# Performance work log

Measured on AMD Instinct MI355X. Metric: run time of the kernel, lower is better.

The kernel has to match this reference:

```python
import jax, jax.numpy as jnp
import numpy as np
import math

IMAGE_SIZE = 256
N_ANGLES = 180


def setup_inputs() -> dict:
    key = jax.random.key(0)
    x = jax.random.normal(key, (4, 1, IMAGE_SIZE, IMAGE_SIZE), dtype=jnp.float32)
    return {"x": x}


def reference(x) -> jnp.ndarray:
    # Radon transform, circle=True: mask to inscribed circle, then for each
    # angle bilinearly sample the image along rotated coordinates
    # (torch.grid_sample, align_corners=True, zeros padding) and sum along rays.
    B = x.shape[0]
    S = IMAGE_SIZE
    A = N_ANGLES
    img = x.reshape(B, S, S)

    # circular mask (matches torch: sqrt(dist2) <= center with center = S//2)
    center = S // 2
    yy, xx = jnp.meshgrid(jnp.arange(S), jnp.arange(S), indexing='ij')
    dist = jnp.sqrt(((xx - center) ** 2 + (yy - center) ** 2).astype(jnp.float32))
    img = img * (dist <= center).astype(img.dtype)
    img_flat = img.reshape(B, S * S)

    # projection coordinates: meshgrid('ij') of linspace(-S/2, S/2, S)
    lin = jnp.linspace(-S / 2.0, S / 2.0, S, dtype=jnp.float32)
    X, Y = jnp.meshgrid(lin, lin, indexing='ij')  # [S,S]; X varies along i
    Xf, Yf = X.ravel(), Y.ravel()                 # [S*S]

    # all rotation angles at once: torch.linspace(0, 180, A) degrees
    ang = jnp.linspace(0.0, 180.0, A, dtype=jnp.float32) * (math.pi / 180.0)
    c = jnp.cos(ang)[:, None]  # [A,1]
    s = jnp.sin(ang)[:, None]
    half = S / 2.0
    gx = (c * Xf - s * Yf) / half  # [A, S*S], normalized grid x (width)
    gy = (s * Xf + c * Yf) / half  # [A, S*S], normalized grid y (height)

    # align_corners=True: pixel = (g + 1)/2 * (S - 1)
    px = (gx + 1.0) * 0.5 * (S - 1)
    py = (gy + 1.0) * 0.5 * (S - 1)

    x0 = jnp.floor(px)
    y0 = jnp.floor(py)
    wx = px - x0
    wy = py - y0
    x0i = x0.astype(jnp.int32)
    y0i = y0.astype(jnp.int32)
    x1i = x0i + 1
    y1i = y0i + 1

    def corner(xi, yi, w):
        # zeros padding: out-of-bounds corners contribute 0
        valid = (xi >= 0) & (xi < S) & (yi >= 0) & (yi < S)
        idx = jnp.clip(yi, 0, S - 1) * S + jnp.clip(xi, 0, S - 1)  # [A, S*S]
        vals = jnp.take(img_flat, idx, axis=1)                      # [B, A, S*S]
        return vals * (w * valid.astype(img.dtype))

    acc = (corner(x0i, y0i, (1.0 - wx) * (1.0 - wy))
           + corner(x1i, y0i, wx * (1.0 - wy))
           + corner(x0i, y1i, (1.0 - wx) * wy)
           + corner(x1i, y1i, wx * wy))  # [B, A, S*S]

    # flat order is (i, j) from meshgrid('ij'); torch sums over output H == i
    sinogram = acc.reshape(B, A, S, S).sum(axis=2)  # [B, A, S]
    return sinogram
```

## Files before the change

### kernel.cpp

```cpp
#include <hip/hip_runtime.h>
#include <hip/hip_fp16.h>
#include <math.h>

#define S 256
#define A 180
#define B 4
#define NSLOT 18285

__global__ void radon_mask_pack(const float* __restrict__ in, uint* __restrict__ ws,
                                float* __restrict__ osino) {
    int idx = blockIdx.x * 256 + threadIdx.x;
    if (idx < 2 * S * S) {
        int c = idx >> 16;
        int p = idx & 65535;
        int y = p >> 8;
        int x = p & 255;
        int dx = x - 128, dy = y - 128;
        bool inside = (dx * dx + dy * dy <= 16384);
        float v0 = in[(2 * c) * (S * S) + p];
        float v1 = in[(2 * c + 1) * (S * S) + p];
        v0 = inside ? v0 : 0.0f;
        v1 = inside ? v1 : 0.0f;
        uint lo = (uint)__half_as_ushort(__float2half(v0));
        uint hi = (uint)__half_as_ushort(__float2half(v1));
        ws[c * (S * S) + p] = lo | (hi << 16);
    }
    if (idx < A * B * S) osino[idx] = 0.0f;
}

__global__ __launch_bounds__(1024, 8) void radon_lds_kernel(const uint* __restrict__ ws,
                                                            float* __restrict__ out) {
    __shared__ uint lds[NSLOT];

    const int a = blockIdx.x;
    const int c = blockIdx.y;
    const int g = blockIdx.z;
    const int tid = threadIdx.x;

    float ang = (float)a * (float)(M_PI / 179.0);
    float sn, cs;
    sincosf(ang, &sn, &cs);

    const bool ymode = (fabsf(sn) >= fabsf(cs));
    const float rate = ymode ? sn : cs;
    const int wstart = 64 * g - 2;
    const int st = ymode ? 265 : 69;

    {
        const uint* __restrict__ src = ws + c * (S * S);
        if (ymode) {
#pragma unroll
            for (int it = 0; it < 18; ++it) {
                int p = it * 1024 + tid;
                if (p < 69 * 264) {
                    int r = p / 264;
                    int c2 = p - r * 264;
                    int y = wstart + r;
                    int x = c2 - 4;
                    uint d = 0u;
                    if (((unsigned)y < 256u) && ((unsigned)x < 256u)) d = src[y * 256 + x];
                    lds[r * 265 + c2] = d;
                }
            }
        } else {
#pragma unroll
            for (int it = 0; it < 18; ++it) {
                int p = it * 1024 + tid;
                if (p < 264 * 69) {
                    int r = p / 69;
                    int c2 = p - r * 69;
                    int y = r - 4;
                    int x = wstart + c2;
                    uint d = 0u;
                    if (((unsigned)y < 256u) && ((unsigned)x < 256u)) d = src[y * 256 + x];
                    lds[p] = d;
                }
            }
        }
    }
    __syncthreads();

    const int j = tid >> 2;
    const int q = tid & 3;

    const float ry = (float)j - 127.5f;
    const float bx = fmaf(-sn, ry, 127.5f);
    const float by = fmaf(cs, ry, 127.5f);
    const float ry2 = ry * ry;

    float hd = sqrtf(16934.0f - ry2);
    int ilo = max((int)ceilf(127.5f - hd), 0);
    int ihi = min((int)floorf(127.5f + hd) + 1, S);

    const float w0 = ymode ? by : bx;
    float invr = 1.0f / rate;
    bool neg = (rate < 0.0f);
    float cLo, cHi;
    if (!neg) {
        cLo = (g == 0) ? -1.0f : (float)(64 * g);
        cHi = (g == 3) ? 256.0f : (float)(64 * g + 64);
    } else {
        cLo = (g == 3) ? 256.0f : (float)(64 * g + 64);
        cHi = (g == 0) ? -1.0f : (float)(64 * g);
    }
    int FLo = (int)fminf(fmaxf(ceilf(127.5f + (cLo - w0) * invr), 0.0f), 256.0f);
    int FHi = (int)fminf(fmaxf(ceilf(127.5f + (cHi - w0) * invr), 0.0f), 256.0f);
    int lo0 = max(ilo, FLo);
    int hi0 = min(ihi, FHi);
    int len = max(hi0 - lo0, 0);
    int lo = lo0 + ((q * len) >> 2);
    int hi = lo0 + (((q + 1) * len) >> 2);

    const float bxp = fmaf(-127.5f, cs, bx) + (ymode ? 4.0f : (float)(-wstart));
    const float byl = fmaf(-127.5f, sn, by) + (ymode ? (float)(-wstart) : 4.0f);

    __half2 acc2 = __floats2half2_rn(0.0f, 0.0f);

#pragma unroll 4
    for (int i = lo; i < hi; ++i) {
        float fi = (float)i;
        float px = fmaf(cs, fi, bxp);
        float py = fmaf(sn, fi, byl);

        float x0f = floorf(px);
        float y0f = floorf(py);
        float wx = px - x0f;
        float wy = py - y0f;
        int xl = (int)x0f;
        int yl = (int)y0f;
        int addr = yl * st + xl;

        uint d00 = lds[addr];
        uint d10 = lds[addr + 1];
        uint d01 = lds[addr + st];
        uint d11 = lds[addr + st + 1];

        __half2 h00 = __builtin_bit_cast(__half2, d00);
        __half2 h10 = __builtin_bit_cast(__half2, d10);
        __half2 h01 = __builtin_bit_cast(__half2, d01);
        __half2 h11 = __builtin_bit_cast(__half2, d11);

        __half2 wxh = __float2half2_rn(wx);
        __half2 wyh = __float2half2_rn(wy);

        __half2 r0 = __hfma2(wxh, __hsub2(h10, h00), h00);
        __half2 r1 = __hfma2(wxh, __hsub2(h11, h01), h01);
        acc2 = __hfma2(wyh, __hsub2(r1, r0), __hadd2(acc2, r0));
    }

    float accA = __half2float(__low2half(acc2));
    float accB = __half2float(__high2half(acc2));

    accA += __shfl_xor(accA, 1, 64);
    accB += __shfl_xor(accB, 1, 64);
    accA += __shfl_xor(accA, 2, 64);
    accB += __shfl_xor(accB, 2, 64);
    if (q == 0) {
        size_t o = ((size_t)(2 * c) * A + a) * S + j;
        atomicAdd(&out[o], accA);
        atomicAdd(&out[o + (size_t)A * S], accB);
    }
}

extern "C" void kernel_launch(void* const* d_in, const int* in_sizes, int n_in,
                              void* d_out, int out_size, void* d_ws, size_t ws_size,
                              hipStream_t stream) {
    const float* x = (const float*)d_in[0];
    float* out = (float*)d_out;
    uint* ws = (uint*)d_ws;

    radon_mask_pack<<<dim3(720), dim3(256), 0, stream>>>(x, ws, out);
    radon_lds_kernel<<<dim3(A, 2, 4), dim3(1024), 0, stream>>>(ws, out);
}
```

Before: 88.46 us.

## Pack all four batch images into uint2 and process them in one block

The pack kernel now stores all four batch images as four fp16 values in a uint2 per pixel. The main kernel loads this uint2 tile into LDS and interpolates all four images per sample, so the grid's batch-pair dimension drops from 2 to 1. Coordinate, weight and address computation is shared across all batches, and there are half as many blocks. LDS per block doubles (about 146KB), which limits occupancy and may exceed the LDS available, and the launch bound drops to 4.

```diff
diff --git a/kernel.cpp b/kernel.cpp
--- a/kernel.cpp
+++ b/kernel.cpp
@@ -7,33 +7,32 @@
 #define B 4
 #define NSLOT 18285
 
-__global__ void radon_mask_pack(const float* __restrict__ in, uint* __restrict__ ws,
+__global__ void radon_mask_pack(const float* __restrict__ in, uint2* __restrict__ ws,
                                 float* __restrict__ osino) {
     int idx = blockIdx.x * 256 + threadIdx.x;
-    if (idx < 2 * S * S) {
-        int c = idx >> 16;
-        int p = idx & 65535;
-        int y = p >> 8;
-        int x = p & 255;
+    if (idx < S * S) {
+        int y = idx >> 8;
+        int x = idx & 255;
         int dx = x - 128, dy = y - 128;
         bool inside = (dx * dx + dy * dy <= 16384);
-        float v0 = in[(2 * c) * (S * S) + p];
-        float v1 = in[(2 * c + 1) * (S * S) + p];
-        v0 = inside ? v0 : 0.0f;
-        v1 = inside ? v1 : 0.0f;
-        uint lo = (uint)__half_as_ushort(__float2half(v0));
-        uint hi = (uint)__half_as_ushort(__float2half(v1));
-        ws[c * (S * S) + p] = lo | (hi << 16);
+        float v0 = inside ? in[idx] : 0.0f;
+        float v1 = inside ? in[S * S + idx] : 0.0f;
+        float v2 = inside ? in[2 * S * S + idx] : 0.0f;
+        float v3 = inside ? in[3 * S * S + idx] : 0.0f;
+        uint lo = (uint)__half_as_ushort(__float2half(v0)) |
+                  ((uint)__half_as_ushort(__float2half(v1)) << 16);
+        uint hi = (uint)__half_as_ushort(__float2half(v2)) |
+                  ((uint)__half_as_ushort(__float2half(v3)) << 16);
+        ws[idx] = make_uint2(lo, hi);
     }
     if (idx < A * B * S) osino[idx] = 0.0f;
 }
 
-__global__ __launch_bounds__(1024, 8) void radon_lds_kernel(const uint* __restrict__ ws,
+__global__ __launch_bounds__(1024, 4) void radon_lds_kernel(const uint2* __restrict__ ws,
                                                             float* __restrict__ out) {
-    __shared__ uint lds[NSLOT];
+    __shared__ uint2 lds2[NSLOT];
 
     const int a = blockIdx.x;
-    const int c = blockIdx.y;
     const int g = blockIdx.z;
     const int tid = threadIdx.x;
 
@@ -46,35 +45,32 @@
     const int wstart = 64 * g - 2;
     const int st = ymode ? 265 : 69;
 
-    {
-        const uint* __restrict__ src = ws + c * (S * S);
-        if (ymode) {
+    if (ymode) {
 #pragma unroll
-            for (int it = 0; it < 18; ++it) {
-                int p = it * 1024 + tid;
-                if (p < 69 * 264) {
-                    int r = p / 264;
-                    int c2 = p - r * 264;
-                    int y = wstart + r;
-                    int x = c2 - 4;
-                    uint d = 0u;
-                    if (((unsigned)y < 256u) && ((unsigned)x < 256u)) d = src[y * 256 + x];
-                    lds[r * 265 + c2] = d;
-                }
+        for (int it = 0; it < 18; ++it) {
+            int p = it * 1024 + tid;
+            if (p < 69 * 264) {
+                int r = p / 264;
+                int c2 = p - r * 264;
+                int y = wstart + r;
+                int x = c2 - 4;
+                uint2 d = make_uint2(0u, 0u);
+                if (((unsigned)y < 256u) && ((unsigned)x < 256u)) d = ws[y * 256 + x];
+                lds2[r * 265 + c2] = d;
             }
-        } else {
+        }
+    } else {
 #pragma unroll
-            for (int it = 0; it < 18; ++it) {
-                int p = it * 1024 + tid;
-                if (p < 264 * 69) {
-                    int r = p / 69;
-                    int c2 = p - r * 69;
-                    int y = r - 4;
-                    int x = wstart + c2;
-                    uint d = 0u;
-                    if (((unsigned)y < 256u) && ((unsigned)x < 256u)) d = src[y * 256 + x];
-                    lds[p] = d;
-                }
+        for (int it = 0; it < 18; ++it) {
+            int p = it * 1024 + tid;
+            if (p < 264 * 69) {
+                int r = p / 69;
+                int c2 = p - r * 69;
+                int y = r - 4;
+                int x = wstart + c2;
+                uint2 d = make_uint2(0u, 0u);
+                if (((unsigned)y < 256u) && ((unsigned)x < 256u)) d = ws[y * 256 + x];
+                lds2[p] = d;
             }
         }
     }
@@ -114,7 +110,8 @@
     const float bxp = fmaf(-127.5f, cs, bx) + (ymode ? 4.0f : (float)(-wstart));
     const float byl = fmaf(-127.5f, sn, by) + (ymode ? (float)(-wstart) : 4.0f);
 
-    __half2 acc2 = __floats2half2_rn(0.0f, 0.0f);
+    __half2 accP = __floats2half2_rn(0.0f, 0.0f);
+    __half2 accQ = __floats2half2_rn(0.0f, 0.0f);
 
 #pragma unroll 4
     for (int i = lo; i < hi; ++i) {
@@ -130,35 +127,47 @@
         int yl = (int)y0f;
         int addr = yl * st + xl;
 
-        uint d00 = lds[addr];
-        uint d10 = lds[addr + 1];
-        uint d01 = lds[addr + st];
-        uint d11 = lds[addr + st + 1];
-
-        __half2 h00 = __builtin_bit_cast(__half2, d00);
-        __half2 h10 = __builtin_bit_cast(__half2, d10);
-        __half2 h01 = __builtin_bit_cast(__half2, d01);
-        __half2 h11 = __builtin_bit_cast(__half2, d11);
+        uint2 d00 = lds2[addr];
+        uint2 d10 = lds2[addr + 1];
+        uint2 d01 = lds2[addr + st];
+        uint2 d11 = lds2[addr + st + 1];
 
         __half2 wxh = __float2half2_rn(wx);
         __half2 wyh = __float2half2_rn(wy);
 
-        __half2 r0 = __hfma2(wxh, __hsub2(h10, h00), h00);
-        __half2 r1 = __hfma2(wxh, __hsub2(h11, h01), h01);
-        acc2 = __hfma2(wyh, __hsub2(r1, r0), __hadd2(acc2, r0));
+        __half2 p00 = __builtin_bit_cast(__half2, d00.x);
+        __half2 p10 = __builtin_bit_cast(__half2, d10.x);
+        __half2 p01 = __builtin_bit_cast(__half2, d01.x);
+        __half2 p11 = __builtin_bit_cast(__half2, d11.x);
+        __half2 r0 = __hfma2(wxh, __hsub2(p10, p00), p00);
+        __half2 r1 = __hfma2(wxh, __hsub2(p11, p01), p01);
+        accP = __hfma2(wyh, __hsub2(r1, r0), __hadd2(accP, r0));
+
+        __half2 s00 = __builtin_bit_cast(__half2, d00.y);
+        __half2 s10 = __builtin_bit_cast(__half2, d10.y);
+        __half2 s01 = __builtin_bit_cast(__half2, d01.y);
+        __half2 s11 = __builtin_bit_cast(__half2, d11.y);
+        __half2 t0 = __hfma2(wxh, __hsub2(s10, s00), s00);
+        __half2 t1 = __hfma2(wxh, __hsub2(s11, s01), s01);
+        accQ = __hfma2(wyh, __hsub2(t1, t0), __hadd2(accQ, t0));
     }
 
-    float accA = __half2float(__low2half(acc2));
-    float accB = __half2float(__high2half(acc2));
+    float a0 = __half2float(__low2half(accP));
+    float a1 = __half2float(__high2half(accP));
+    float a2 = __half2float(__low2half(accQ));
+    float a3 = __half2float(__high2half(accQ));
 
-    accA += __shfl_xor(accA, 1, 64);
-    accB += __shfl_xor(accB, 1, 64);
-    accA += __shfl_xor(accA, 2, 64);
-    accB += __shfl_xor(accB, 2, 64);
+    a0 += __shfl_xor(a0, 1, 64);  a1 += __shfl_xor(a1, 1, 64);
+    a2 += __shfl_xor(a2, 1, 64);  a3 += __shfl_xor(a3, 1, 64);
+    a0 += __shfl_xor(a0, 2, 64);  a1 += __shfl_xor(a1, 2, 64);
+    a2 += __shfl_xor(a2, 2, 64);  a3 += __shfl_xor(a3, 2, 64);
     if (q == 0) {
-        size_t o = ((size_t)(2 * c) * A + a) * S + j;
-        atomicAdd(&out[o], accA);
-        atomicAdd(&out[o + (size_t)A * S], accB);
+        size_t o = (size_t)a * S + j;
+        const size_t stride = (size_t)A * S;
+        atomicAdd(&out[o], a0);
+        atomicAdd(&out[o + stride], a1);
+        atomicAdd(&out[o + 2 * stride], a2);
+        atomicAdd(&out[o + 3 * stride], a3);
     }
 }
 
@@ -167,8 +176,8 @@
                               hipStream_t stream) {
     const float* x = (const float*)d_in[0];
     float* out = (float*)d_out;
-    uint* ws = (uint*)d_ws;
+    uint2* ws = (uint2*)d_ws;
 
     radon_mask_pack<<<dim3(720), dim3(256), 0, stream>>>(x, ws, out);
-    radon_lds_kernel<<<dim3(A, 2, 4), dim3(1024), 0, stream>>>(ws, out);
+    radon_lds_kernel<<<dim3(A, 1, 4), dim3(1024), 0, stream>>>(ws, out);
 }
```

Measured after the change: 85.95 us. -2.8%, faster.
